# Optimization experiments

Hardware: AMD Instinct MI355X
Metric: run time of the kernel (lower is better)

## Reference

```python
import jax, jax.numpy as jnp
import numpy as np

KERNEL = 31
GROUPS = 8
EPS = 1e-5


def mha1d(x, Wq, Wk, Wv, rel):
    """Sliding-window multi-head attention (MutliHeadAttention1D).
    x: [b, s, in_f]; Wq/Wk/Wv: [out_f, in_f] (torch Linear layout); rel: [1, out_f, KERNEL].
    Returns (out [b, s, out_f], attn [b, s, GROUPS, KERNEL])."""
    b, s, _ = x.shape
    out_f = Wq.shape[0]
    d = out_f // GROUPS
    pad = (KERNEL - 1) // 2
    xp = jnp.pad(x, ((0, 0), (pad, pad), (0, 0)))
    q = jnp.einsum('bsf,of->bso', x, Wq)          # [b, s, out_f]
    k = jnp.einsum('bsf,of->bso', xp, Wk)         # [b, s+2*pad, out_f]
    v = jnp.einsum('bsf,of->bso', xp, Wv)
    # unfold: window index [s, KERNEL]
    idx = jnp.arange(s)[:, None] + jnp.arange(KERNEL)[None, :]
    kw = jnp.swapaxes(k[:, idx], 2, 3) + rel       # [b, s, out_f, KERNEL]
    vw = jnp.swapaxes(v[:, idx], 2, 3)             # [b, s, out_f, KERNEL]
    kw = kw.reshape(b, s, GROUPS, d, KERNEL)
    vw = vw.reshape(b, s, GROUPS, d, KERNEL)
    qh = q.reshape(b, s, GROUPS, d, 1)
    energy = jnp.sum(qh * kw, axis=-2, keepdims=True)   # [b, s, g, 1, K]
    attn = jax.nn.softmax(energy, axis=-1)               # [b, s, g, 1, K]
    out = jnp.sum(attn * vw, axis=-1).reshape(b, s, out_f)
    return out, attn[:, :, :, 0, :]


def layer_norm(x, g, b):
    mu = jnp.mean(x, axis=-1, keepdims=True)
    var = jnp.mean(jnp.square(x - mu), axis=-1, keepdims=True)
    return (x - mu) / jnp.sqrt(var + EPS) * g + b


def setup_inputs() -> dict:
    key = jax.random.key(0)
    ks = jax.random.split(key, 20)
    in_f, mc, out_f = 229, 48, 88
    d = {}
    d['spec'] = jax.random.normal(ks[0], (8, 8192, in_f), dtype=jnp.float32)
    # onset attention block (in 229 -> 48)
    d['Wq1'] = jax.random.normal(ks[1], (mc, in_f), dtype=jnp.float32) * 0.1
    d['Wk1'] = jax.random.normal(ks[2], (mc, in_f), dtype=jnp.float32) * 0.1
    d['Wv1'] = jax.random.normal(ks[3], (mc, in_f), dtype=jnp.float32) * 0.1
    d['rel1'] = jax.random.normal(ks[4], (1, mc, KERNEL), dtype=jnp.float32)
    d['ln1_g'] = jnp.ones((mc,), jnp.float32)
    d['ln1_b'] = jnp.zeros((mc,), jnp.float32)
    d['Wo'] = jax.random.normal(ks[5], (out_f, mc), dtype=jnp.float32) * 0.1
    d['bo'] = jnp.zeros((out_f,), jnp.float32)
    # frame attention block (in 48+88=136 -> 48)
    in2 = mc + out_f
    d['Wq2'] = jax.random.normal(ks[6], (mc, in2), dtype=jnp.float32) * 0.1
    d['Wk2'] = jax.random.normal(ks[7], (mc, in2), dtype=jnp.float32) * 0.1
    d['Wv2'] = jax.random.normal(ks[8], (mc, in2), dtype=jnp.float32) * 0.1
    d['rel2'] = jax.random.normal(ks[9], (1, mc, KERNEL), dtype=jnp.float32)
    d['ln2_g'] = jnp.ones((mc,), jnp.float32)
    d['ln2_b'] = jnp.zeros((mc,), jnp.float32)
    d['Wf'] = jax.random.normal(ks[10], (out_f, mc), dtype=jnp.float32) * 0.1
    d['bf'] = jnp.zeros((out_f,), jnp.float32)
    return d


def reference(spec, Wq1, Wk1, Wv1, rel1, ln1_g, ln1_b, Wo, bo,
              Wq2, Wk2, Wv2, rel2, ln2_g, ln2_b, Wf, bf):
    x, a = mha1d(spec, Wq1, Wk1, Wv1, rel1)
    x = layer_norm(x, ln1_g, ln1_b)
    onset_pred = jax.nn.sigmoid(jnp.einsum('bsm,om->bso', x, Wo) + bo)
    x = jnp.concatenate((onset_pred, x), axis=-1)
    x, _ = mha1d(x, Wq2, Wk2, Wv2, rel2)
    x = layer_norm(x, ln2_g, ln2_b)
    frame_pred = jax.nn.sigmoid(jnp.einsum('bsm,om->bso', x, Wf) + bf)
    return frame_pred, onset_pred, a
```

## Files before the change

kernel.cpp:

```cpp
#include <hip/hip_runtime.h>
#include <math.h>

namespace {

constexpr int B_   = 8;
constexpr int S_   = 8192;
constexpr int NROW = B_ * S_;
constexpr int MC   = 48;
constexpr int OF   = 88;
constexpr int KW   = 31;
constexpr int F1   = 229;
constexpr int F2   = 136;

typedef __attribute__((ext_vector_type(8))) short bf16x8;
typedef __attribute__((ext_vector_type(4))) float f32x4;

__device__ inline unsigned short f2bf(float v) {
    unsigned u = __float_as_uint(v);
    unsigned r = (u + 0x7FFFu + ((u >> 16) & 1u)) >> 16;
    return (unsigned short)r;
}
__device__ inline float bf2f(unsigned short b) {
    return __uint_as_float((unsigned)b << 16);
}
__device__ inline unsigned pack2(unsigned short a, unsigned short b) {
    return (unsigned)a | ((unsigned)b << 16);
}

__global__ void wprep_kernel(const float* __restrict__ Wq,
                             const float* __restrict__ Wk,
                             const float* __restrict__ Wv,
                             int K, int nch, unsigned short* __restrict__ out) {
    int idx = blockIdx.x * 256 + threadIdx.x;
    int kpad = nch * 32;
    int total = 144 * kpad;
    if (idx >= total) return;
    int oc = idx / kpad;
    int kg = idx - oc * kpad;
    int c  = kg >> 5, kk = kg & 31;
    float val = 0.f;
    if (kg < K) {
        const float* W = (oc < 48) ? Wq : (oc < 96 ? Wk : Wv);
        int ocl = (oc < 48) ? oc : (oc < 96 ? oc - 48 : oc - 96);
        val = W[ocl * K + kg];
    }
    unsigned short h = f2bf(val);
    unsigned short l = f2bf(val - bf2f(h));
    size_t base = (size_t)c * 9216 + (size_t)((kk >> 3) * 144 + oc) * 8 + (kk & 7);
    out[base]        = h;
    out[base + 4608] = l;
}

__global__ void woprep_kernel(const float* __restrict__ W,
                              unsigned short* __restrict__ out) {
    int idx = blockIdx.x * 256 + threadIdx.x;
    if (idx >= 96 * 64) return;
    int n = idx >> 6, k = idx & 63;
    float val = (n < OF && k < MC) ? W[n * MC + k] : 0.f;
    unsigned short h = f2bf(val);
    unsigned short l = f2bf(val - bf2f(h));
    out[idx]        = h;
    out[6144 + idx] = l;
}

template<int K, int NCH>
__global__ __launch_bounds__(256, 3) void proj_mfma(
    const float* __restrict__ x,
    const unsigned short* __restrict__ wbuf,
    float* __restrict__ qo, float* __restrict__ ko, float* __restrict__ vo)
{
    const int tid  = threadIdx.x;
    const int row0 = blockIdx.x * 64;
    const int lane = tid & 63;
    const int wm   = tid >> 6;
    const int lr   = lane & 15;
    const int hig  = lane >> 4;
    const int arow = wm * 16 + lr;

    const float* xrow = x + (size_t)(row0 + arow) * K;
    const unsigned short* wl = wbuf + (size_t)(hig * 144 + lr) * 8;

    f32x4 acc[9];
    #pragma unroll
    for (int nt = 0; nt < 9; ++nt) acc[nt] = f32x4{0.f, 0.f, 0.f, 0.f};

    for (int c = 0; c < NCH; ++c) {
        const int k0 = c * 32 + hig * 8;
        float av[8];
        #pragma unroll
        for (int u = 0; u < 8; ++u)
            av[u] = (k0 + u < K) ? xrow[k0 + u] : 0.f;

        const unsigned short* wc = wl + (size_t)c * 9216;
        bf16x8 bh[9], bl[9];
        #pragma unroll
        for (int nt = 0; nt < 9; ++nt) {
            bh[nt] = *(const bf16x8*)&wc[nt * 128];
            bl[nt] = *(const bf16x8*)&wc[4608 + nt * 128];
        }
        __builtin_amdgcn_sched_barrier(0);

        union { bf16x8 v; unsigned u[4]; } ah, al;
        #pragma unroll
        for (int p = 0; p < 4; ++p) {
            unsigned short h0 = f2bf(av[2 * p]);
            unsigned short h1 = f2bf(av[2 * p + 1]);
            ah.u[p] = pack2(h0, h1);
            al.u[p] = pack2(f2bf(av[2 * p]     - bf2f(h0)),
                            f2bf(av[2 * p + 1] - bf2f(h1)));
        }

        #pragma unroll
        for (int nt = 0; nt < 9; ++nt) {
            acc[nt] = __builtin_amdgcn_mfma_f32_16x16x32_bf16(ah.v, bh[nt], acc[nt], 0, 0, 0);
            acc[nt] = __builtin_amdgcn_mfma_f32_16x16x32_bf16(ah.v, bl[nt], acc[nt], 0, 0, 0);
            acc[nt] = __builtin_amdgcn_mfma_f32_16x16x32_bf16(al.v, bh[nt], acc[nt], 0, 0, 0);
        }
    }

    const int orow = row0 + wm * 16 + (hig << 2);
    #pragma unroll
    for (int nt = 0; nt < 9; ++nt) {
        float* dst = (nt < 3) ? qo : (nt < 6 ? ko : vo);
        int oc = (nt % 3) * 16 + lr;
        #pragma unroll
        for (int rg = 0; rg < 4; ++rg)
            dst[(size_t)(orow + rg) * MC + oc] = acc[nt][rg];
    }
}

template<bool FIRST>
__global__ __launch_bounds__(512, 6) void attn_core(
    const float* __restrict__ qb,
    const float* __restrict__ kb,
    const float* __restrict__ vb,
    const float* __restrict__ rel,
    const float* __restrict__ lng,
    const float* __restrict__ lnb,
    float* __restrict__ attn_out,
    float* __restrict__ x2)
{
    __shared__ __attribute__((aligned(16))) float ks[94 * 52];
    __shared__ __attribute__((aligned(16))) float vs[94 * 52];
    __shared__ __attribute__((aligned(16))) float relT[31 * 52];
    __shared__ float lngs[48], lnbs[48];

    const int tid = threadIdx.x;
    const int bid = ((blockIdx.x & 7) << 7) | (blockIdx.x >> 3);
    const int bb  = bid >> 7;
    const int st0 = (bid & 127) * 64;
    const size_t base = (size_t)bb * S_;

    for (int idx = tid; idx < 94 * 12; idx += 512) {
        int rr = idx / 12, c4 = idx - rr * 12;
        int si = st0 - 15 + rr;
        float4 k4 = {0.f, 0.f, 0.f, 0.f}, v4 = {0.f, 0.f, 0.f, 0.f};
        if (si >= 0 && si < S_) {
            k4 = *(const float4*)&kb[(base + si) * MC + c4 * 4];
            v4 = *(const float4*)&vb[(base + si) * MC + c4 * 4];
        }
        *(float4*)&ks[rr * 52 + c4 * 4] = k4;
        *(float4*)&vs[rr * 52 + c4 * 4] = v4;
    }
    for (int idx = tid; idx < MC * KW; idx += 512) {
        int c = idx / KW, j = idx - c * KW;
        relT[j * 52 + c] = rel[idx];
    }
    if (tid < 48) { lngs[tid] = lng[tid]; lnbs[tid] = lnb[tid]; }
    __syncthreads();

    const int rl  = tid >> 3;
    const int g   = tid & 7;
    const int ch0 = g * 6;
    const size_t grow = base + st0 + rl;

    const float* qr = qb + grow * MC + ch0;
    float2 q01 = *(const float2*)(qr);
    float2 q23 = *(const float2*)(qr + 2);
    float2 q45 = *(const float2*)(qr + 4);

    float e[KW];
    #pragma unroll
    for (int j = 0; j < KW; ++j) {
        const float* rp = &relT[j * 52 + ch0];
        float2 r01 = *(const float2*)(rp);
        float2 r23 = *(const float2*)(rp + 2);
        float2 r45 = *(const float2*)(rp + 4);
        e[j] = q01.x * r01.x + q01.y * r01.y + q23.x * r23.x
             + q23.y * r23.y + q45.x * r45.x + q45.y * r45.y;
    }
    float mx = -1e30f;
    #pragma unroll
    for (int j = 0; j < KW; ++j) {
        const float* kp = &ks[(rl + j) * 52 + ch0];
        float2 k01 = *(const float2*)(kp);
        float2 k23 = *(const float2*)(kp + 2);
        float2 k45 = *(const float2*)(kp + 4);
        float s = e[j] + q01.x * k01.x + q01.y * k01.y + q23.x * k23.x
                       + q23.y * k23.y + q45.x * k45.x + q45.y * k45.y;
        e[j] = s;
        mx = fmaxf(mx, s);
    }
    float den = 0.f;
    #pragma unroll
    for (int j = 0; j < KW; ++j) { float t = __expf(e[j] - mx); e[j] = t; den += t; }
    float rden = 1.f / den;

    float o0 = 0.f, o1 = 0.f, o2 = 0.f, o3 = 0.f, o4 = 0.f, o5 = 0.f;
    float* aout = FIRST ? (attn_out + (grow * 8 + g) * KW) : nullptr;
    #pragma unroll
    for (int j = 0; j < KW; ++j) {
        float aw = e[j] * rden;
        if constexpr (FIRST) aout[j] = aw;
        const float* vp = &vs[(rl + j) * 52 + ch0];
        float2 v01 = *(const float2*)(vp);
        float2 v23 = *(const float2*)(vp + 2);
        float2 v45 = *(const float2*)(vp + 4);
        o0 += aw * v01.x; o1 += aw * v01.y; o2 += aw * v23.x;
        o3 += aw * v23.y; o4 += aw * v45.x; o5 += aw * v45.y;
    }

    float sum = o0 + o1 + o2 + o3 + o4 + o5;
    sum += __shfl_xor(sum, 1, 8);
    sum += __shfl_xor(sum, 2, 8);
    sum += __shfl_xor(sum, 4, 8);
    float mu = sum * (1.f / 48.f);
    float d0 = o0 - mu, d1 = o1 - mu, d2 = o2 - mu, d3 = o3 - mu, d4 = o4 - mu, d5 = o5 - mu;
    float vr = d0*d0 + d1*d1 + d2*d2 + d3*d3 + d4*d4 + d5*d5;
    vr += __shfl_xor(vr, 1, 8);
    vr += __shfl_xor(vr, 2, 8);
    vr += __shfl_xor(vr, 4, 8);
    float rstd = rsqrtf(vr * (1.f / 48.f) + 1e-5f);

    float* xp = x2 + grow * F2 + OF + ch0;
    *(float2*)(xp)     = float2{d0 * rstd * lngs[ch0]     + lnbs[ch0],
                                d1 * rstd * lngs[ch0 + 1] + lnbs[ch0 + 1]};
    *(float2*)(xp + 2) = float2{d2 * rstd * lngs[ch0 + 2] + lnbs[ch0 + 2],
                                d3 * rstd * lngs[ch0 + 3] + lnbs[ch0 + 3]};
    *(float2*)(xp + 4) = float2{d4 * rstd * lngs[ch0 + 4] + lnbs[ch0 + 4],
                                d5 * rstd * lngs[ch0 + 5] + lnbs[ch0 + 5]};
}

template<bool FIRST>
__global__ __launch_bounds__(256, 4) void pred_gemm(
    const float* x2,
    const unsigned short* __restrict__ wop,
    const float* __restrict__ bo,
    float* __restrict__ pred,
    float* x2w)
{
    __shared__ __attribute__((aligned(16))) unsigned short yh[64 * 72];
    __shared__ __attribute__((aligned(16))) unsigned short yl[64 * 72];
    __shared__ float bosL[96];

    const int tid  = threadIdx.x;
    const int row0 = blockIdx.x * 64;

    for (int idx = tid; idx < 768; idx += 256) {
        int r = idx / 12, c4 = idx - r * 12;
        float4 v4 = *(const float4*)&x2[(size_t)(row0 + r) * F2 + OF + c4 * 4];
        unsigned short h0 = f2bf(v4.x), h1 = f2bf(v4.y), h2 = f2bf(v4.z), h3 = f2bf(v4.w);
        unsigned short l0 = f2bf(v4.x - bf2f(h0)), l1 = f2bf(v4.y - bf2f(h1));
        unsigned short l2 = f2bf(v4.z - bf2f(h2)), l3 = f2bf(v4.w - bf2f(h3));
        *(uint2*)&yh[r * 72 + c4 * 4] = uint2{pack2(h0, h1), pack2(h2, h3)};
        *(uint2*)&yl[r * 72 + c4 * 4] = uint2{pack2(l0, l1), pack2(l2, l3)};
    }
    for (int idx = tid; idx < 384; idx += 256) {
        int r = idx / 6, u = idx - r * 6;
        *(uint2*)&yh[r * 72 + 48 + u * 4] = uint2{0u, 0u};
        *(uint2*)&yl[r * 72 + 48 + u * 4] = uint2{0u, 0u};
    }
    if (tid < 96) bosL[tid] = (tid < OF) ? bo[tid] : 0.f;
    __syncthreads();

    const int l   = tid & 63;
    const int w   = tid >> 6;
    const int lr  = l & 15;
    const int lk8 = (l >> 4) * 8;

    const int arow = w * 16 + lr;
    bf16x8 ah0 = *(const bf16x8*)&yh[arow * 72 + lk8];
    bf16x8 al0 = *(const bf16x8*)&yl[arow * 72 + lk8];
    bf16x8 ah1 = *(const bf16x8*)&yh[arow * 72 + 32 + lk8];
    bf16x8 al1 = *(const bf16x8*)&yl[arow * 72 + 32 + lk8];

    const int rowo = row0 + w * 16 + ((l >> 4) << 2);
    #pragma unroll
    for (int nt = 0; nt < 6; ++nt) {
        int ncol = nt * 16 + lr;
        bf16x8 bh0 = *(const bf16x8*)&wop[(size_t)ncol * 64 + lk8];
        bf16x8 bl0 = *(const bf16x8*)&wop[6144 + (size_t)ncol * 64 + lk8];
        bf16x8 bh1 = *(const bf16x8*)&wop[(size_t)ncol * 64 + 32 + lk8];
        bf16x8 bl1 = *(const bf16x8*)&wop[6144 + (size_t)ncol * 64 + 32 + lk8];
        f32x4 oacc = f32x4{0.f, 0.f, 0.f, 0.f};
        oacc = __builtin_amdgcn_mfma_f32_16x16x32_bf16(ah0, bh0, oacc, 0, 0, 0);
        oacc = __builtin_amdgcn_mfma_f32_16x16x32_bf16(ah0, bl0, oacc, 0, 0, 0);
        oacc = __builtin_amdgcn_mfma_f32_16x16x32_bf16(al0, bh0, oacc, 0, 0, 0);
        oacc = __builtin_amdgcn_mfma_f32_16x16x32_bf16(ah1, bh1, oacc, 0, 0, 0);
        oacc = __builtin_amdgcn_mfma_f32_16x16x32_bf16(ah1, bl1, oacc, 0, 0, 0);
        oacc = __builtin_amdgcn_mfma_f32_16x16x32_bf16(al1, bh1, oacc, 0, 0, 0);
        if (ncol < OF) {
            float bias = bosL[ncol];
            #pragma unroll
            for (int rg = 0; rg < 4; ++rg) {
                float s  = oacc[rg] + bias;
                float sg = 1.f / (1.f + __expf(-s));
                size_t row = (size_t)(rowo + rg);
                pred[row * OF + ncol] = sg;
                if constexpr (FIRST) x2w[row * F2 + ncol] = sg;
            }
        }
    }
}

}

extern "C" void kernel_launch(void* const* d_in, const int* in_sizes, int n_in,
                              void* d_out, int out_size, void* d_ws, size_t ws_size,
                              hipStream_t stream) {
    const float* spec = (const float*)d_in[0];
    const float* Wq1  = (const float*)d_in[1];
    const float* Wk1  = (const float*)d_in[2];
    const float* Wv1  = (const float*)d_in[3];
    const float* rel1 = (const float*)d_in[4];
    const float* ln1g = (const float*)d_in[5];
    const float* ln1b = (const float*)d_in[6];
    const float* Wo   = (const float*)d_in[7];
    const float* bo   = (const float*)d_in[8];
    const float* Wq2  = (const float*)d_in[9];
    const float* Wk2  = (const float*)d_in[10];
    const float* Wv2  = (const float*)d_in[11];
    const float* rel2 = (const float*)d_in[12];
    const float* ln2g = (const float*)d_in[13];
    const float* ln2b = (const float*)d_in[14];
    const float* Wf   = (const float*)d_in[15];
    const float* bf_  = (const float*)d_in[16];

    float* outf   = (float*)d_out;
    float* frame  = outf;
    float* onset  = outf + (size_t)NROW * OF;
    float* attn_a = outf + (size_t)2 * NROW * OF;

    float* wsf = (float*)d_ws;
    float* q1 = wsf;
    float* k1 = q1 + (size_t)NROW * MC;
    float* v1 = k1 + (size_t)NROW * MC;
    float* x2 = v1 + (size_t)NROW * MC;
    unsigned short* wbuf1 = (unsigned short*)(x2 + (size_t)NROW * F2);
    unsigned short* wbuf2 = wbuf1 + (size_t)8 * 9216;
    unsigned short* woP1  = wbuf2 + (size_t)5 * 9216;
    unsigned short* woP2  = woP1 + 2 * 6144;

    wprep_kernel<<<(144 * 8 * 32 + 255) / 256, 256, 0, stream>>>(Wq1, Wk1, Wv1, F1, 8, wbuf1);
    wprep_kernel<<<(144 * 5 * 32 + 255) / 256, 256, 0, stream>>>(Wq2, Wk2, Wv2, F2, 5, wbuf2);
    woprep_kernel<<<24, 256, 0, stream>>>(Wo, woP1);
    woprep_kernel<<<24, 256, 0, stream>>>(Wf, woP2);

    proj_mfma<F1, 8><<<NROW / 64, 256, 0, stream>>>(spec, wbuf1, q1, k1, v1);
    attn_core<true><<<NROW / 64, 512, 0, stream>>>(q1, k1, v1, rel1, ln1g, ln1b,
                                                   attn_a, x2);
    pred_gemm<true><<<NROW / 64, 256, 0, stream>>>(x2, woP1, bo, onset, x2);
    proj_mfma<F2, 5><<<NROW / 64, 256, 0, stream>>>(x2, wbuf2, q1, k1, v1);
    attn_core<false><<<NROW / 64, 512, 0, stream>>>(q1, k1, v1, rel2, ln2g, ln2b,
                                                    nullptr, x2);
    pred_gemm<false><<<NROW / 64, 256, 0, stream>>>(x2, woP2, bf_, frame, nullptr);
}
```

Baseline: 192.5 us.

## Pre-pack projection inputs into MFMA-fragment bf16 hi/lo layout

Adds a packA kernel that converts the spectrogram into bf16 hi/lo split planes laid out in MFMA A-fragment order, and has pred_gemm<true> emit the second projection's input directly in that packed form instead of a float x2 buffer. proj_mfma now loads ready-made bf16x8 fragments instead of doing strided scalar float loads and per-chunk conversion. The goal is coalesced A loads and less conversion ALU inside the GEMM. The cost is an extra launch plus a round trip of packed data, which is the same byte count as fp32 (two bf16 planes) but written once more for stage 1.

```diff
diff --git a/kernel.cpp b/kernel.cpp
--- a/kernel.cpp
+++ b/kernel.cpp
@@ -11,6 +11,10 @@
 constexpr int KW   = 31;
 constexpr int F1   = 229;
 constexpr int F2   = 136;
+constexpr int NCH1 = 8;
+constexpr int NCH2 = 5;
+constexpr size_t PLANE1 = (size_t)(NROW / 16) * NCH1 * 512;
+constexpr size_t PLANE2 = (size_t)(NROW / 16) * NCH2 * 512;
 
 typedef __attribute__((ext_vector_type(8))) short bf16x8;
 typedef __attribute__((ext_vector_type(4))) float f32x4;
@@ -63,21 +67,55 @@
     out[6144 + idx] = l;
 }
 
-template<int K, int NCH>
+__global__ __launch_bounds__(256) void packA_kernel(
+    const float* __restrict__ x,
+    unsigned short* __restrict__ out)
+{
+    __shared__ float xs[32][260];
+    const int tid  = threadIdx.x;
+    const int row0 = blockIdx.x * 32;
+
+    for (int idx = tid; idx < 32 * 256; idx += 256) {
+        int r = idx >> 8, kk = idx & 255;
+        xs[r][kk] = (kk < F1) ? x[(size_t)(row0 + r) * F1 + kk] : 0.f;
+    }
+    __syncthreads();
+
+    const int tt   = tid >> 7;
+    const int j    = tid & 127;
+    const int lane = j >> 1;
+    const int half = j & 1;
+    const int lr   = lane & 15;
+    const int hig  = lane >> 4;
+    const size_t T0 = (size_t)(row0 >> 4);
+
+    #pragma unroll
+    for (int c = 0; c < NCH1; ++c) {
+        float4 v = *(const float4*)&xs[tt * 16 + lr][c * 32 + hig * 8 + half * 4];
+        unsigned short h0 = f2bf(v.x), h1 = f2bf(v.y), h2 = f2bf(v.z), h3 = f2bf(v.w);
+        uint2 hh = uint2{pack2(h0, h1), pack2(h2, h3)};
+        uint2 ll = uint2{pack2(f2bf(v.x - bf2f(h0)), f2bf(v.y - bf2f(h1))),
+                         pack2(f2bf(v.z - bf2f(h2)), f2bf(v.w - bf2f(h3)))};
+        size_t off = (((T0 + tt) * NCH1 + c) * 64 + lane) * 8 + half * 4;
+        *(uint2*)&out[off]          = hh;
+        *(uint2*)&out[PLANE1 + off] = ll;
+    }
+}
+
+template<int NCH, size_t PLANE>
 __global__ __launch_bounds__(256, 3) void proj_mfma(
-    const float* __restrict__ x,
+    const unsigned short* __restrict__ apack,
     const unsigned short* __restrict__ wbuf,
     float* __restrict__ qo, float* __restrict__ ko, float* __restrict__ vo)
 {
     const int tid  = threadIdx.x;
-    const int row0 = blockIdx.x * 64;
     const int lane = tid & 63;
     const int wm   = tid >> 6;
     const int lr   = lane & 15;
     const int hig  = lane >> 4;
-    const int arow = wm * 16 + lr;
-
-    const float* xrow = x + (size_t)(row0 + arow) * K;
+    const size_t t = (size_t)blockIdx.x * 4 + wm;
+
+    const unsigned short* ap = apack + (t * NCH) * 512 + (size_t)lane * 8;
     const unsigned short* wl = wbuf + (size_t)(hig * 144 + lr) * 8;
 
     f32x4 acc[9];
@@ -85,12 +123,8 @@
     for (int nt = 0; nt < 9; ++nt) acc[nt] = f32x4{0.f, 0.f, 0.f, 0.f};
 
     for (int c = 0; c < NCH; ++c) {
-        const int k0 = c * 32 + hig * 8;
-        float av[8];
-        #pragma unroll
-        for (int u = 0; u < 8; ++u)
-            av[u] = (k0 + u < K) ? xrow[k0 + u] : 0.f;
-
+        bf16x8 ah = *(const bf16x8*)&ap[c * 512];
+        bf16x8 al = *(const bf16x8*)&ap[PLANE + c * 512];
         const unsigned short* wc = wl + (size_t)c * 9216;
         bf16x8 bh[9], bl[9];
         #pragma unroll
@@ -99,26 +133,15 @@
             bl[nt] = *(const bf16x8*)&wc[4608 + nt * 128];
         }
         __builtin_amdgcn_sched_barrier(0);
-
-        union { bf16x8 v; unsigned u[4]; } ah, al;
-        #pragma unroll
-        for (int p = 0; p < 4; ++p) {
-            unsigned short h0 = f2bf(av[2 * p]);
-            unsigned short h1 = f2bf(av[2 * p + 1]);
-            ah.u[p] = pack2(h0, h1);
-            al.u[p] = pack2(f2bf(av[2 * p]     - bf2f(h0)),
-                            f2bf(av[2 * p + 1] - bf2f(h1)));
-        }
-
         #pragma unroll
         for (int nt = 0; nt < 9; ++nt) {
-            acc[nt] = __builtin_amdgcn_mfma_f32_16x16x32_bf16(ah.v, bh[nt], acc[nt], 0, 0, 0);
-            acc[nt] = __builtin_amdgcn_mfma_f32_16x16x32_bf16(ah.v, bl[nt], acc[nt], 0, 0, 0);
-            acc[nt] = __builtin_amdgcn_mfma_f32_16x16x32_bf16(al.v, bh[nt], acc[nt], 0, 0, 0);
+            acc[nt] = __builtin_amdgcn_mfma_f32_16x16x32_bf16(ah, bh[nt], acc[nt], 0, 0, 0);
+            acc[nt] = __builtin_amdgcn_mfma_f32_16x16x32_bf16(ah, bl[nt], acc[nt], 0, 0, 0);
+            acc[nt] = __builtin_amdgcn_mfma_f32_16x16x32_bf16(al, bh[nt], acc[nt], 0, 0, 0);
         }
     }
 
-    const int orow = row0 + wm * 16 + (hig << 2);
+    const int orow = blockIdx.x * 64 + wm * 16 + (hig << 2);
     #pragma unroll
     for (int nt = 0; nt < 9; ++nt) {
         float* dst = (nt < 3) ? qo : (nt < 6 ? ko : vo);
@@ -138,7 +161,7 @@
     const float* __restrict__ lng,
     const float* __restrict__ lnb,
     float* __restrict__ attn_out,
-    float* __restrict__ x2)
+    float* __restrict__ y1)
 {
     __shared__ __attribute__((aligned(16))) float ks[94 * 52];
     __shared__ __attribute__((aligned(16))) float vs[94 * 52];
@@ -232,25 +255,27 @@
     vr += __shfl_xor(vr, 4, 8);
     float rstd = rsqrtf(vr * (1.f / 48.f) + 1e-5f);
 
-    float* xp = x2 + grow * F2 + OF + ch0;
-    *(float2*)(xp)     = float2{d0 * rstd * lngs[ch0]     + lnbs[ch0],
+    float* yp = y1 + grow * MC + ch0;
+    *(float2*)(yp)     = float2{d0 * rstd * lngs[ch0]     + lnbs[ch0],
                                 d1 * rstd * lngs[ch0 + 1] + lnbs[ch0 + 1]};
-    *(float2*)(xp + 2) = float2{d2 * rstd * lngs[ch0 + 2] + lnbs[ch0 + 2],
+    *(float2*)(yp + 2) = float2{d2 * rstd * lngs[ch0 + 2] + lnbs[ch0 + 2],
                                 d3 * rstd * lngs[ch0 + 3] + lnbs[ch0 + 3]};
-    *(float2*)(xp + 4) = float2{d4 * rstd * lngs[ch0 + 4] + lnbs[ch0 + 4],
+    *(float2*)(yp + 4) = float2{d4 * rstd * lngs[ch0 + 4] + lnbs[ch0 + 4],
                                 d5 * rstd * lngs[ch0 + 5] + lnbs[ch0 + 5]};
 }
 
 template<bool FIRST>
-__global__ __launch_bounds__(256, 4) void pred_gemm(
-    const float* x2,
+__global__ __launch_bounds__(256) void pred_gemm(
+    const float* __restrict__ y1,
     const unsigned short* __restrict__ wop,
     const float* __restrict__ bo,
     float* __restrict__ pred,
-    float* x2w)
+    unsigned short* __restrict__ a2)
 {
     __shared__ __attribute__((aligned(16))) unsigned short yh[64 * 72];
     __shared__ __attribute__((aligned(16))) unsigned short yl[64 * 72];
+    __shared__ unsigned short sgh[FIRST ? 64 * 100 : 1];
+    __shared__ unsigned short sgl[FIRST ? 64 * 100 : 1];
     __shared__ float bosL[96];
 
     const int tid  = threadIdx.x;
@@ -258,7 +283,7 @@
 
     for (int idx = tid; idx < 768; idx += 256) {
         int r = idx / 12, c4 = idx - r * 12;
-        float4 v4 = *(const float4*)&x2[(size_t)(row0 + r) * F2 + OF + c4 * 4];
+        float4 v4 = *(const float4*)&y1[(size_t)(row0 + r) * MC + c4 * 4];
         unsigned short h0 = f2bf(v4.x), h1 = f2bf(v4.y), h2 = f2bf(v4.z), h3 = f2bf(v4.w);
         unsigned short l0 = f2bf(v4.x - bf2f(h0)), l1 = f2bf(v4.y - bf2f(h1));
         unsigned short l2 = f2bf(v4.z - bf2f(h2)), l3 = f2bf(v4.w - bf2f(h3));
@@ -284,7 +309,7 @@
     bf16x8 ah1 = *(const bf16x8*)&yh[arow * 72 + 32 + lk8];
     bf16x8 al1 = *(const bf16x8*)&yl[arow * 72 + 32 + lk8];
 
-    const int rowo = row0 + w * 16 + ((l >> 4) << 2);
+    const int lrow0 = w * 16 + ((l >> 4) << 2);
     #pragma unroll
     for (int nt = 0; nt < 6; ++nt) {
         int ncol = nt * 16 + lr;
@@ -305,10 +330,38 @@
             for (int rg = 0; rg < 4; ++rg) {
                 float s  = oacc[rg] + bias;
                 float sg = 1.f / (1.f + __expf(-s));
-                size_t row = (size_t)(rowo + rg);
-                pred[row * OF + ncol] = sg;
-                if constexpr (FIRST) x2w[row * F2 + ncol] = sg;
+                pred[(size_t)(row0 + lrow0 + rg) * OF + ncol] = sg;
+                if constexpr (FIRST) {
+                    unsigned short h = f2bf(sg);
+                    sgh[(lrow0 + rg) * 100 + ncol] = h;
+                    sgl[(lrow0 + rg) * 100 + ncol] = f2bf(sg - bf2f(h));
+                }
             }
+        }
+    }
+
+    if constexpr (FIRST) {
+        __syncthreads();
+        const int tt2 = tid >> 6, lane2 = tid & 63;
+        const int lr2 = lane2 & 15, hig2 = lane2 >> 4;
+        const int row = tt2 * 16 + lr2;
+        const size_t T0 = (size_t)blockIdx.x * 4;
+        #pragma unroll
+        for (int c = 0; c < NCH2; ++c) {
+            unsigned short h8[8], l8[8];
+            #pragma unroll
+            for (int u = 0; u < 8; ++u) {
+                int k = c * 32 + hig2 * 8 + u;
+                unsigned short hv = 0, lv = 0;
+                if (k < OF)       { hv = sgh[row * 100 + k];      lv = sgl[row * 100 + k]; }
+                else if (k < F2)  { hv = yh[row * 72 + (k - OF)]; lv = yl[row * 72 + (k - OF)]; }
+                h8[u] = hv; l8[u] = lv;
+            }
+            size_t off = ((T0 + tt2) * NCH2 + c) * 512 + (size_t)lane2 * 8;
+            *(uint4*)&a2[off] = uint4{pack2(h8[0], h8[1]), pack2(h8[2], h8[3]),
+                                      pack2(h8[4], h8[5]), pack2(h8[6], h8[7])};
+            *(uint4*)&a2[PLANE2 + off] = uint4{pack2(l8[0], l8[1]), pack2(l8[2], l8[3]),
+                                               pack2(l8[4], l8[5]), pack2(l8[6], l8[7])};
         }
     }
 }
@@ -345,23 +398,26 @@
     float* q1 = wsf;
     float* k1 = q1 + (size_t)NROW * MC;
     float* v1 = k1 + (size_t)NROW * MC;
-    float* x2 = v1 + (size_t)NROW * MC;
-    unsigned short* wbuf1 = (unsigned short*)(x2 + (size_t)NROW * F2);
-    unsigned short* wbuf2 = wbuf1 + (size_t)8 * 9216;
-    unsigned short* woP1  = wbuf2 + (size_t)5 * 9216;
+    float* y1 = v1 + (size_t)NROW * MC;
+    unsigned short* A1 = (unsigned short*)(y1 + (size_t)NROW * MC);
+    unsigned short* A2 = A1;
+    unsigned short* wbuf1 = A1 + 2 * PLANE1;
+    unsigned short* wbuf2 = wbuf1 + (size_t)NCH1 * 9216;
+    unsigned short* woP1  = wbuf2 + (size_t)NCH2 * 9216;
     unsigned short* woP2  = woP1 + 2 * 6144;
 
-    wprep_kernel<<<(144 * 8 * 32 + 255) / 256, 256, 0, stream>>>(Wq1, Wk1, Wv1, F1, 8, wbuf1);
-    wprep_kernel<<<(144 * 5 * 32 + 255) / 256, 256, 0, stream>>>(Wq2, Wk2, Wv2, F2, 5, wbuf2);
+    wprep_kernel<<<(144 * NCH1 * 32 + 255) / 256, 256, 0, stream>>>(Wq1, Wk1, Wv1, F1, NCH1, wbuf1);
+    wprep_kernel<<<(144 * NCH2 * 32 + 255) / 256, 256, 0, stream>>>(Wq2, Wk2, Wv2, F2, NCH2, wbuf2);
     woprep_kernel<<<24, 256, 0, stream>>>(Wo, woP1);
     woprep_kernel<<<24, 256, 0, stream>>>(Wf, woP2);
 
-    proj_mfma<F1, 8><<<NROW / 64, 256, 0, stream>>>(spec, wbuf1, q1, k1, v1);
+    packA_kernel<<<NROW / 32, 256, 0, stream>>>(spec, A1);
+    proj_mfma<NCH1, PLANE1><<<NROW / 64, 256, 0, stream>>>(A1, wbuf1, q1, k1, v1);
     attn_core<true><<<NROW / 64, 512, 0, stream>>>(q1, k1, v1, rel1, ln1g, ln1b,
-                                                   attn_a, x2);
-    pred_gemm<true><<<NROW / 64, 256, 0, stream>>>(x2, woP1, bo, onset, x2);
-    proj_mfma<F2, 5><<<NROW / 64, 256, 0, stream>>>(x2, wbuf2, q1, k1, v1);
+                                                   attn_a, y1);
+    pred_gemm<true><<<NROW / 64, 256, 0, stream>>>(y1, woP1, bo, onset, A2);
+    proj_mfma<NCH2, PLANE2><<<NROW / 64, 256, 0, stream>>>(A2, wbuf2, q1, k1, v1);
     attn_core<false><<<NROW / 64, 512, 0, stream>>>(q1, k1, v1, rel2, ln2g, ln2b,
-                                                    nullptr, x2);
-    pred_gemm<false><<<NROW / 64, 256, 0, stream>>>(x2, woP2, bf_, frame, nullptr);
-}
+                                                    nullptr, y1);
+    pred_gemm<false><<<NROW / 64, 256, 0, stream>>>(y1, woP2, bf_, frame, A2);
+}
```

Measured after the change: 237.3 us. 1.23x slower.
